# Kernel tuning notes

Measured on AMD Instinct MI355X. Metric: run time of the kernel, lower is better.

## Reference

```python
import jax, jax.numpy as jnp
import numpy as np

EPS = 1e-5

def _conv1x1(x, W, b):
    # x: [B,Ci,H,W], W: [Co,Ci]
    return jnp.einsum('oi,bihw->bohw', W, x) + b[None, :, None, None]

def _bn(x, gamma, beta, mean, var):
    # inference-mode BatchNorm2d
    s = gamma / jnp.sqrt(var + EPS)
    return x * s[None, :, None, None] + (beta - mean * s)[None, :, None, None]

def _conv3x3(x, W, b):
    y = jax.lax.conv_general_dilated(x, W, (1, 1), 'SAME',
                                     dimension_numbers=('NCHW', 'OIHW', 'NCHW'))
    return y + b[None, :, None, None]

def _sparsemax_last(S):
    # sparsemax over the last axis (TrackHSPA: max-subtract, sort, cumsum, threshold)
    S = S - jnp.max(S, axis=-1, keepdims=True)
    srt = -jnp.sort(-S, axis=-1)                 # descending sort
    csum = jnp.cumsum(srt, axis=-1) - 1.0
    N = S.shape[-1]
    ar = jnp.arange(1, N + 1, dtype=S.dtype)
    mask = ar * srt > csum
    k = jnp.sum(mask, axis=-1, keepdims=True)    # support size per row
    tau = jnp.take_along_axis(csum, k - 1, axis=-1) / k.astype(S.dtype)
    return jnp.maximum(S - tau, 0.0)

def _forward(zf, xf, Wq, bq, Ws, bs, Wg, bg, g_gamma, g_beta, g_mean, g_var,
             Wfi, bfi, fi_gamma, fi_beta, fi_mean, fi_var,
             Wm, bm, m_gamma, m_beta, m_mean, m_var, prelu_a):
    B, C, Hx, Wx = xf.shape
    # ---- Graph_Attention_Union (cross-attention) ----
    xf_t = _conv1x1(xf, Wq, bq).reshape(B, C, -1)      # [B,C,Nx]
    zf_t = _conv1x1(zf, Ws, bs).reshape(B, C, -1)      # [B,C,Nz]
    xf_g = jax.nn.relu(_bn(_conv1x1(xf, Wg, bg), g_gamma, g_beta, g_mean, g_var))
    zf_g = jax.nn.relu(_bn(_conv1x1(zf, Wg, bg), g_gamma, g_beta, g_mean, g_var))
    sim = jnp.einsum('bcn,bcm->bnm', xf_t, zf_t)       # [B,Nx,Nz]
    attn = jax.nn.softmax(sim, axis=2)
    emb = jnp.einsum('bcm,bnm->bcn', zf_g.reshape(B, C, -1), attn)
    emb = emb.reshape(B, C, Hx, Wx)
    gat = jax.nn.relu(_bn(_conv1x1(jnp.concatenate([emb, xf_g], axis=1), Wfi, bfi),
                          fi_gamma, fi_beta, fi_mean, fi_var))
    # ---- TrackHSPA (adaptive sparsemax self-attention) ----
    e = _conv3x3(gat, Wm, bm)
    e = _bn(e, m_gamma, m_beta, m_mean, m_var)
    e = jnp.where(e >= 0, e, prelu_a * e)              # PReLU (single param)
    N = Hx * Wx
    ef = e.reshape(B, -1, N)                           # [B,C',N]
    S = jnp.einsum('bdi,bdj->bij', ef, ef)             # [B,N,N]
    P = _sparsemax_last(S)
    out = jnp.einsum('bcn,bnm->bcm', gat.reshape(B, C, N), P)
    return out.reshape(B, C, Hx, Wx) + gat


def setup_inputs():
    key = jax.random.key(0)
    ks = jax.random.split(key, 8)
    B, C, Hz, Wz, Hx, Wx = 32, 256, 7, 7, 31, 31
    Cm = C // 4
    f = lambda k, shape: jax.random.normal(k, shape, jnp.float32) * 0.05
    return {
        'zf': jax.random.normal(ks[0], (B, C, Hz, Wz), jnp.float32),
        'xf': jax.random.normal(ks[1], (B, C, Hx, Wx), jnp.float32),
        'Wq': f(ks[2], (C, C)), 'bq': jnp.zeros((C,), jnp.float32),
        'Ws': f(ks[3], (C, C)), 'bs': jnp.zeros((C,), jnp.float32),
        'Wg': f(ks[4], (C, C)), 'bg': jnp.zeros((C,), jnp.float32),
        'g_gamma': jnp.ones((C,), jnp.float32), 'g_beta': jnp.zeros((C,), jnp.float32),
        'g_mean': jnp.zeros((C,), jnp.float32), 'g_var': jnp.ones((C,), jnp.float32),
        'Wfi': f(ks[5], (C, 2 * C)), 'bfi': jnp.zeros((C,), jnp.float32),
        'fi_gamma': jnp.ones((C,), jnp.float32), 'fi_beta': jnp.zeros((C,), jnp.float32),
        'fi_mean': jnp.zeros((C,), jnp.float32), 'fi_var': jnp.ones((C,), jnp.float32),
        'Wm': f(ks[6], (Cm, C, 3, 3)), 'bm': jnp.zeros((Cm,), jnp.float32),
        'm_gamma': jnp.ones((Cm,), jnp.float32), 'm_beta': jnp.zeros((Cm,), jnp.float32),
        'm_mean': jnp.zeros((Cm,), jnp.float32), 'm_var': jnp.ones((Cm,), jnp.float32),
        'prelu_a': jnp.array(0.25, jnp.float32),
    }


def reference(zf, xf, Wq, bq, Ws, bs, Wg, bg, g_gamma, g_beta, g_mean, g_var,
              Wfi, bfi, fi_gamma, fi_beta, fi_mean, fi_var,
              Wm, bm, m_gamma, m_beta, m_mean, m_var, prelu_a):
    return _forward(zf, xf, Wq, bq, Ws, bs, Wg, bg, g_gamma, g_beta, g_mean, g_var,
                    Wfi, bfi, fi_gamma, fi_beta, fi_mean, fi_var,
                    Wm, bm, m_gamma, m_beta, m_mean, m_var, prelu_a)
```

## Files before the change

### kernel.cpp

```cpp
#include <hip/hip_runtime.h>
#include <cstdint>
#include <cstddef>
#include <math.h>

typedef __attribute__((ext_vector_type(8))) short short8;
typedef __attribute__((ext_vector_type(4))) float floatx4;
typedef unsigned short ushort_t;

__device__ __forceinline__ ushort_t f2bf(float x) {
    union { float f; unsigned u; } v; v.f = x;
    unsigned r = v.u + 0x7FFF + ((v.u >> 16) & 1);
    return (ushort_t)(r >> 16);
}
__device__ __forceinline__ float bf2f(ushort_t h) {
    union { unsigned u; float f; } v; v.u = ((unsigned)h) << 16; return v.f;
}
__device__ __forceinline__ void split2(float v, ushort_t& h, ushort_t& l) {
    h = f2bf(v);
    l = f2bf(v - bf2f(h));
}

#define MFMA(a, b, c) __builtin_amdgcn_mfma_f32_16x16x32_bf16((a), (b), (c), 0, 0, 0)

__device__ __forceinline__ void gload_lds16(const void* g, void* l) {
    __builtin_amdgcn_global_load_lds(
        (const __attribute__((address_space(1))) unsigned*)g,
        (__attribute__((address_space(3))) unsigned*)l, 16, 0, 0);
}

__global__ void prep_all_kernel(
    const float* __restrict__ Wq, const float* __restrict__ Ws,
    const float* __restrict__ Wg, const float* __restrict__ Wfi,
    const float* __restrict__ Wm,
    const float* bq, const float* bs,
    const float* bg, const float* gg, const float* gb, const float* gm, const float* gv,
    const float* bfi, const float* fg, const float* fb, const float* fm, const float* fv,
    const float* bm, const float* mg, const float* mb, const float* mm, const float* mv,
    ushort_t* Wq_h, ushort_t* Wq_l, ushort_t* Ws_h, ushort_t* Ws_l,
    ushort_t* Wg_h, ushort_t* Wg_l, ushort_t* Wfi_h, ushort_t* Wfi_l,
    ushort_t* wm_h, ushort_t* wm_l, float* scsh)
{
    int bid = blockIdx.x, t = threadIdx.x;
    if (bid < 256) {
        int i = bid * 256 + t; ushort_t h, l; split2(Wq[i], h, l); Wq_h[i] = h; Wq_l[i] = l;
    } else if (bid < 512) {
        int i = (bid - 256) * 256 + t; ushort_t h, l; split2(Ws[i], h, l); Ws_h[i] = h; Ws_l[i] = l;
    } else if (bid < 768) {
        int i = (bid - 512) * 256 + t; ushort_t h, l; split2(Wg[i], h, l); Wg_h[i] = h; Wg_l[i] = l;
    } else if (bid < 1280) {
        int i = (bid - 768) * 256 + t; ushort_t h, l; split2(Wfi[i], h, l); Wfi_h[i] = h; Wfi_l[i] = l;
    } else if (bid < 1856) {
        int i = (bid - 1280) * 256 + t;
        int c = i & 255, m = (i >> 8) & 63, tap = i >> 14;
        ushort_t h, l; split2(Wm[((size_t)m * 256 + c) * 9 + tap], h, l);
        wm_h[i] = h; wm_l[i] = l;
    } else {
        if (t < 256) {
            scsh[t] = 1.f;        scsh[256 + t] = bq[t];
            scsh[512 + t] = 1.f;  scsh[768 + t] = bs[t];
            float s = gg[t] * rsqrtf(gv[t] + 1e-5f);
            scsh[1024 + t] = s;   scsh[1280 + t] = gb[t] + s * (bg[t] - gm[t]);
            float s2 = fg[t] * rsqrtf(fv[t] + 1e-5f);
            scsh[1536 + t] = s2;  scsh[1792 + t] = fb[t] + s2 * (bfi[t] - fm[t]);
            if (t < 64) {
                float s3 = mg[t] * rsqrtf(mv[t] + 1e-5f);
                scsh[2048 + t] = s3; scsh[2112 + t] = mb[t] + s3 * (bm[t] - mm[t]);
            }
        }
    }
}

__global__ void halo_zero_kernel(ushort_t* __restrict__ gxh, ushort_t* __restrict__ gxl) {
    int i = blockIdx.x * 256 + threadIdx.x;
    int b = i >> 7, k = i & 127;
    int r;
    if (k < 33) r = k;
    else if (k < 66) r = 32 * 33 + (k - 33);
    else { int k2 = k - 66; r = ((k2 >> 1) + 1) * 33 + ((k2 & 1) ? 32 : 0); }
    uint4* ph = (uint4*)(gxh + ((size_t)b * 1089 + r) * 256);
    uint4* pl = (uint4*)(gxl + ((size_t)b * 1089 + r) * 256);
    uint4 z = make_uint4(0, 0, 0, 0);
#pragma unroll
    for (int s = 0; s < 32; s++) { ph[s] = z; pl[s] = z; }
}

__global__ __launch_bounds__(256) void transpose_in_kernel(
    const float* __restrict__ in, ushort_t* __restrict__ oh, ushort_t* __restrict__ ol,
    int Nsrc, int Npad)
{
    int b = blockIdx.z;
    const float* ib = in + (size_t)b * 256 * Nsrc;
    ushort_t* obh = oh + (size_t)b * Npad * 256;
    ushort_t* obl = ol + (size_t)b * Npad * 256;
    __shared__ float tile[32][33];
    int n0 = blockIdx.x * 32, c0 = blockIdx.y * 32;
    int tx = threadIdx.x & 31, ty = threadIdx.x >> 5;
#pragma unroll
    for (int r = 0; r < 4; r++) {
        int c = c0 + ty + r * 8, n = n0 + tx;
        tile[ty + r * 8][tx] = (n < Nsrc) ? ib[(size_t)c * Nsrc + n] : 0.f;
    }
    __syncthreads();
#pragma unroll
    for (int r = 0; r < 4; r++) {
        int n = n0 + ty + r * 8, c = c0 + tx;
        if (n < Nsrc) {
            ushort_t h, l; split2(tile[tx][ty + r * 8], h, l);
            obh[(size_t)n * 256 + c] = h;
            obl[(size_t)n * 256 + c] = l;
        }
    }
}

__global__ __launch_bounds__(256, 2) void dualconv_mfma_kernel(
    const ushort_t* __restrict__ Xh, const ushort_t* __restrict__ Xl,
    const ushort_t* __restrict__ W1h, const ushort_t* __restrict__ W1l,
    const ushort_t* __restrict__ W2h, const ushort_t* __restrict__ W2l,
    const float* __restrict__ sc1, const float* __restrict__ sh1,
    const float* __restrict__ sc2, const float* __restrict__ sh2,
    int relu1, int relu2,
    ushort_t* __restrict__ O1h, ushort_t* __restrict__ O1l,
    ushort_t* __restrict__ O2h, ushort_t* __restrict__ O2l,
    ushort_t* __restrict__ O2ch, ushort_t* __restrict__ O2cl, int cpitch,
    int K, int Nvalid, int NpadIn, int NpadOut)
{
    __shared__ ushort_t Bs[16384];
    int b = blockIdx.x;
    int n0 = blockIdx.y * 32;
    const ushort_t* Xbh = Xh + (size_t)b * NpadIn * K;
    const ushort_t* Xbl = Xl + (size_t)b * NpadIn * K;
    int tid = threadIdx.x, w = tid >> 6, l = tid & 63, lc = l & 15, q = l >> 4;
    int m0 = w * 64;

#pragma unroll
    for (int r = 0; r < 8; r++) {
        int d = r * 4096 + w * 1024 + l * 16;
        int seg = d >> 14;
        int dr = d & 16383;
        int row = dr >> 9;
        int inrow = (dr & 511) ^ ((row & 7) << 4);
        int srow = n0 + row; if (srow > NpadIn - 1) srow = NpadIn - 1;
        const ushort_t* src = (seg ? Xbl : Xbh) + (size_t)srow * K + (inrow >> 1);
        char* dst = (char*)Bs + (r * 4096 + w * 1024);
        gload_lds16(src, dst);
    }
    __syncthreads();

#define DC_LOADA(K0, AH, AL) do { \
    _Pragma("unroll") \
    for (int mt_ = 0; mt_ < 4; mt_++) { \
        size_t off_ = (size_t)(m0 + mt_ * 16 + lc) * K + (K0) + q * 8; \
        AH[mt_] = *(const short8*)(Wh + off_); \
        AL[mt_] = *(const short8*)(Wl + off_); \
    } \
} while (0)
#define DC_LDSB(K0, BH, BL) do { \
    _Pragma("unroll") \
    for (int jt_ = 0; jt_ < 2; jt_++) { \
        int row_ = jt_ * 16 + lc; \
        int koff_ = (((K0) + q * 8) * 2) ^ ((row_ & 7) << 4); \
        BH[jt_] = *(const short8*)((const char*)Bs + row_ * 512 + koff_); \
        BL[jt_] = *(const short8*)((const char*)Bs + 16384 + row_ * 512 + koff_); \
    } \
} while (0)
#define DC_MFMA(AH, AL, BH, BL) do { \
    _Pragma("unroll") \
    for (int mt_ = 0; mt_ < 4; mt_++) \
    _Pragma("unroll") \
    for (int jt_ = 0; jt_ < 2; jt_++) { \
        acc[mt_][jt_] = MFMA(AH[mt_], BH[jt_], acc[mt_][jt_]); \
        acc[mt_][jt_] = MFMA(AH[mt_], BL[jt_], acc[mt_][jt_]); \
        acc[mt_][jt_] = MFMA(AL[mt_], BH[jt_], acc[mt_][jt_]); \
    } \
} while (0)

    for (int half = 0; half < 2; half++) {
        const ushort_t* Wh = half ? W2h : W1h;
        const ushort_t* Wl = half ? W2l : W1l;
        const float* sc = half ? sc2 : sc1;
        const float* sh = half ? sh2 : sh1;
        int relu = half ? relu2 : relu1;
        ushort_t* Obh = (half ? O2h : O1h) + (size_t)b * NpadOut * 256;
        ushort_t* Obl = (half ? O2l : O1l) + (size_t)b * NpadOut * 256;

        floatx4 acc[4][2];
#pragma unroll
        for (int i = 0; i < 4; i++)
#pragma unroll
            for (int j = 0; j < 2; j++) acc[i][j] = (floatx4){0.f, 0.f, 0.f, 0.f};

        short8 ah0[4], al0[4], ah1[4], al1[4], bh[2], bl[2];
        DC_LOADA(0, ah0, al0);
        for (int k0 = 0; k0 < K; k0 += 64) {
            DC_LOADA(k0 + 32, ah1, al1);
            DC_LDSB(k0, bh, bl);
            DC_MFMA(ah0, al0, bh, bl);
            if (k0 + 64 < K) DC_LOADA(k0 + 64, ah0, al0);
            DC_LDSB(k0 + 32, bh, bl);
            DC_MFMA(ah1, al1, bh, bl);
        }

#pragma unroll
        for (int mt = 0; mt < 4; mt++) {
            int mb = m0 + mt * 16 + q * 4;
            float s0 = sc[mb], s1 = sc[mb + 1], s2 = sc[mb + 2], s3 = sc[mb + 3];
            float h0 = sh[mb], h1 = sh[mb + 1], h2 = sh[mb + 2], h3 = sh[mb + 3];
#pragma unroll
            for (int jt = 0; jt < 2; jt++) {
                int n = n0 + jt * 16 + lc;
                if (n >= Nvalid) continue;
                float v0 = acc[mt][jt][0] * s0 + h0;
                float v1 = acc[mt][jt][1] * s1 + h1;
                float v2 = acc[mt][jt][2] * s2 + h2;
                float v3 = acc[mt][jt][3] * s3 + h3;
                if (relu) { v0 = fmaxf(v0, 0.f); v1 = fmaxf(v1, 0.f); v2 = fmaxf(v2, 0.f); v3 = fmaxf(v3, 0.f); }
                ushort_t e0, f0, e1, f1, e2, f2, e3, f3;
                split2(v0, e0, f0); split2(v1, e1, f1); split2(v2, e2, f2); split2(v3, e3, f3);
                *(ushort4*)(Obh + (size_t)n * 256 + mb) = make_ushort4(e0, e1, e2, e3);
                *(ushort4*)(Obl + (size_t)n * 256 + mb) = make_ushort4(f0, f1, f2, f3);
                if (half && O2ch) {
                    O2ch[((size_t)b * 256 + mb + 0) * cpitch + n] = e0;
                    O2ch[((size_t)b * 256 + mb + 1) * cpitch + n] = e1;
                    O2ch[((size_t)b * 256 + mb + 2) * cpitch + n] = e2;
                    O2ch[((size_t)b * 256 + mb + 3) * cpitch + n] = e3;
                    O2cl[((size_t)b * 256 + mb + 0) * cpitch + n] = f0;
                    O2cl[((size_t)b * 256 + mb + 1) * cpitch + n] = f1;
                    O2cl[((size_t)b * 256 + mb + 2) * cpitch + n] = f2;
                    O2cl[((size_t)b * 256 + mb + 3) * cpitch + n] = f3;
                }
            }
        }
    }
#undef DC_LOADA
#undef DC_LDSB
#undef DC_MFMA
}

__global__ __launch_bounds__(256) void attn_mfma_kernel(
    const ushort_t* __restrict__ xth, const ushort_t* __restrict__ xtl,
    const ushort_t* __restrict__ zth, const ushort_t* __restrict__ ztl,
    const ushort_t* __restrict__ zgh, const ushort_t* __restrict__ zgl,
    ushort_t* __restrict__ eh, ushort_t* __restrict__ el)
{
    __shared__ float S[64][68];
    __shared__ ushort_t awh[64][72], awl[64][72];
    __shared__ float T[4][16][20];
    int b = blockIdx.x, n0 = blockIdx.y * 64;
    int tid = threadIdx.x, w = tid >> 6, l = tid & 63, lc = l & 15, q = l >> 4;
    const ushort_t* xhb = xth + (size_t)b * 992 * 256;
    const ushort_t* xlb = xtl + (size_t)b * 992 * 256;
    const ushort_t* zhb = zth + (size_t)b * 64 * 256;
    const ushort_t* zlb = ztl + (size_t)b * 64 * 256;
    const ushort_t* ghb = zgh + (size_t)b * 256 * 64;
    const ushort_t* glb = zgl + (size_t)b * 256 * 64;

    int rowg = n0 + w * 16 + lc;
#pragma unroll
    for (int ct = 0; ct < 4; ct++) {
        floatx4 acc = (floatx4){0.f, 0.f, 0.f, 0.f};
        for (int k0 = 0; k0 < 256; k0 += 32) {
            short8 ah = *(const short8*)(xhb + (size_t)rowg * 256 + k0 + q * 8);
            short8 al = *(const short8*)(xlb + (size_t)rowg * 256 + k0 + q * 8);
            short8 bh = *(const short8*)(zhb + (size_t)(ct * 16 + lc) * 256 + k0 + q * 8);
            short8 bl = *(const short8*)(zlb + (size_t)(ct * 16 + lc) * 256 + k0 + q * 8);
            acc = MFMA(ah, bh, acc);
            acc = MFMA(ah, bl, acc);
            acc = MFMA(al, bh, acc);
        }
#pragma unroll
        for (int r = 0; r < 4; r++) S[w * 16 + q * 4 + r][ct * 16 + lc] = acc[r];
    }
    __syncthreads();
    if (tid < 64) {
        float mx = -INFINITY;
        for (int m = 0; m < 49; m++) mx = fmaxf(mx, S[tid][m]);
        float sum = 0.f;
        for (int m = 0; m < 49; m++) { float e = __expf(S[tid][m] - mx); S[tid][m] = e; sum += e; }
        float inv = 1.f / sum;
        for (int m = 0; m < 64; m++) {
            float vv = (m < 49) ? S[tid][m] * inv : 0.f;
            ushort_t hh, ll; split2(vv, hh, ll);
            awh[tid][m] = hh; awl[tid][m] = ll;
        }
    }
    __syncthreads();
    int nw = l >> 2, cg = l & 3;
#pragma unroll
    for (int ct = 0; ct < 16; ct++) {
        floatx4 acc = (floatx4){0.f, 0.f, 0.f, 0.f};
#pragma unroll
        for (int k0 = 0; k0 < 64; k0 += 32) {
            short8 ah = *(const short8*)(&awh[w * 16 + lc][k0 + q * 8]);
            short8 al = *(const short8*)(&awl[w * 16 + lc][k0 + q * 8]);
            short8 bh = *(const short8*)(ghb + (size_t)(ct * 16 + lc) * 64 + k0 + q * 8);
            short8 bl = *(const short8*)(glb + (size_t)(ct * 16 + lc) * 64 + k0 + q * 8);
            acc = MFMA(ah, bh, acc);
            acc = MFMA(ah, bl, acc);
            acc = MFMA(al, bh, acc);
        }
#pragma unroll
        for (int r = 0; r < 4; r++) T[w][q * 4 + r][lc] = acc[r];
        float4 vv = *(const float4*)&T[w][nw][cg * 4];
        int n = n0 + w * 16 + nw;
        if (n < 961) {
            ushort_t h0, l0, h1, l1, h2, l2_, h3, l3;
            split2(vv.x, h0, l0); split2(vv.y, h1, l1);
            split2(vv.z, h2, l2_); split2(vv.w, h3, l3);
            size_t off = ((size_t)b * 992 + n) * 256 + ct * 16 + cg * 4;
            *(ushort4*)(eh + off) = make_ushort4(h0, h1, h2, h3);
            *(ushort4*)(el + off) = make_ushort4(l0, l1, l2_, l3);
        }
    }
}

__global__ __launch_bounds__(256, 2) void fi_mfma_kernel(
    const ushort_t* __restrict__ Eh, const ushort_t* __restrict__ El,
    const ushort_t* __restrict__ Gh, const ushort_t* __restrict__ Gl,
    const ushort_t* __restrict__ Wh, const ushort_t* __restrict__ Wl,
    const float* __restrict__ sc, const float* __restrict__ sh,
    ushort_t* __restrict__ gxh, ushort_t* __restrict__ gxl,
    ushort_t* __restrict__ gat_nf)
{
    __shared__ ushort_t Bs[16384];
    int b = blockIdx.x;
    const ushort_t* Ebh = Eh + (size_t)b * 992 * 256;
    const ushort_t* Ebl = El + (size_t)b * 992 * 256;
    const ushort_t* Gbh = Gh + (size_t)b * 992 * 256;
    const ushort_t* Gbl = Gl + (size_t)b * 992 * 256;
    ushort_t* gxhb = gxh + (size_t)b * 1089 * 256;
    ushort_t* gxlb = gxl + (size_t)b * 1089 * 256;
    ushort_t* gn = gat_nf + (size_t)b * 256 * 992;
    int tid = threadIdx.x, w = tid >> 6, l = tid & 63, lc = l & 15, q = l >> 4;
    int m0 = w * 64, nb0 = blockIdx.y * 32;

    floatx4 acc[4][2];
#pragma unroll
    for (int i = 0; i < 4; i++)
#pragma unroll
        for (int j = 0; j < 2; j++) acc[i][j] = (floatx4){0.f, 0.f, 0.f, 0.f};

#define FI_LOADA(K0, AH, AL) do { \
    _Pragma("unroll") \
    for (int mt_ = 0; mt_ < 4; mt_++) { \
        size_t off_ = (size_t)(m0 + mt_ * 16 + lc) * 512 + (K0) + q * 8; \
        AH[mt_] = *(const short8*)(Wh + off_); \
        AL[mt_] = *(const short8*)(Wl + off_); \
    } \
} while (0)
#define FI_LDSB(K0, BH, BL) do { \
    _Pragma("unroll") \
    for (int jt_ = 0; jt_ < 2; jt_++) { \
        int row_ = jt_ * 16 + lc; \
        int koff_ = (((K0) + q * 8) * 2) ^ ((row_ & 7) << 4); \
        BH[jt_] = *(const short8*)((const char*)Bs + row_ * 512 + koff_); \
        BL[jt_] = *(const short8*)((const char*)Bs + 16384 + row_ * 512 + koff_); \
    } \
} while (0)
#define FI_MFMA(AH, AL, BH, BL) do { \
    _Pragma("unroll") \
    for (int mt_ = 0; mt_ < 4; mt_++) \
    _Pragma("unroll") \
    for (int jt_ = 0; jt_ < 2; jt_++) { \
        acc[mt_][jt_] = MFMA(AH[mt_], BH[jt_], acc[mt_][jt_]); \
        acc[mt_][jt_] = MFMA(AH[mt_], BL[jt_], acc[mt_][jt_]); \
        acc[mt_][jt_] = MFMA(AL[mt_], BH[jt_], acc[mt_][jt_]); \
    } \
} while (0)

    for (int p = 0; p < 2; p++) {
        const ushort_t* srcH = p ? Gbh : Ebh;
        const ushort_t* srcL = p ? Gbl : Ebl;
        if (p) __syncthreads();
#pragma unroll
        for (int r = 0; r < 8; r++) {
            int d = r * 4096 + w * 1024 + l * 16;
            int seg = d >> 14;
            int dr = d & 16383;
            int row = dr >> 9;
            int inrow = (dr & 511) ^ ((row & 7) << 4);
            int srow = nb0 + row; if (srow > 991) srow = 991;
            const ushort_t* src = (seg ? srcL : srcH) + (size_t)srow * 256 + (inrow >> 1);
            char* dst = (char*)Bs + (r * 4096 + w * 1024);
            gload_lds16(src, dst);
        }
        __syncthreads();

        int pb = p * 256;
        short8 ah0[4], al0[4], ah1[4], al1[4], bh[2], bl[2];
        FI_LOADA(pb, ah0, al0);
        for (int kk = 0; kk < 256; kk += 64) {
            FI_LOADA(pb + kk + 32, ah1, al1);
            FI_LDSB(kk, bh, bl);
            FI_MFMA(ah0, al0, bh, bl);
            if (kk + 64 < 256) FI_LOADA(pb + kk + 64, ah0, al0);
            FI_LDSB(kk + 32, bh, bl);
            FI_MFMA(ah1, al1, bh, bl);
        }
    }
#undef FI_LOADA
#undef FI_LDSB
#undef FI_MFMA

#pragma unroll
    for (int mt = 0; mt < 4; mt++) {
        int mb = m0 + mt * 16 + q * 4;
        float s0 = sc[mb], s1 = sc[mb + 1], s2 = sc[mb + 2], s3 = sc[mb + 3];
        float h0 = sh[mb], h1 = sh[mb + 1], h2 = sh[mb + 2], h3 = sh[mb + 3];
#pragma unroll
        for (int jt = 0; jt < 2; jt++) {
            int n = nb0 + jt * 16 + lc;
            if (n >= 961) continue;
            float v0 = fmaxf(acc[mt][jt][0] * s0 + h0, 0.f);
            float v1 = fmaxf(acc[mt][jt][1] * s1 + h1, 0.f);
            float v2 = fmaxf(acc[mt][jt][2] * s2 + h2, 0.f);
            float v3 = fmaxf(acc[mt][jt][3] * s3 + h3, 0.f);
            ushort_t a0, b0, a1, b1, a2, b2, a3, b3;
            split2(v0, a0, b0); split2(v1, a1, b1); split2(v2, a2, b2); split2(v3, a3, b3);
            int hh = n / 31, ww2 = n - hh * 31;
            int row = (hh + 1) * 33 + (ww2 + 1);
            *(ushort4*)(gxhb + (size_t)row * 256 + mb) = make_ushort4(a0, a1, a2, a3);
            *(ushort4*)(gxlb + (size_t)row * 256 + mb) = make_ushort4(b0, b1, b2, b3);
            gn[(size_t)(mb + 0) * 992 + n] = a0;
            gn[(size_t)(mb + 1) * 992 + n] = a1;
            gn[(size_t)(mb + 2) * 992 + n] = a2;
            gn[(size_t)(mb + 3) * 992 + n] = a3;
        }
    }
}

__global__ __launch_bounds__(256, 2) void conv3x3_mfma_kernel(
    const ushort_t* __restrict__ gxh, const ushort_t* __restrict__ gxl,
    const ushort_t* __restrict__ wmh, const ushort_t* __restrict__ wml,
    const float* __restrict__ sc, const float* __restrict__ sh,
    const float* __restrict__ prelu_a,
    ushort_t* __restrict__ eh, ushort_t* __restrict__ el)
{
    __shared__ float Sp[4][2048];
    int b = blockIdx.x;
    const ushort_t* gxhb = gxh + (size_t)b * 1089 * 256;
    const ushort_t* gxlb = gxl + (size_t)b * 1089 * 256;
    ushort_t* ebh = eh + (size_t)b * 1024 * 64;
    ushort_t* ebl = el + (size_t)b * 1024 * 64;
    int tid = threadIdx.x, w = tid >> 6, l = tid & 63, lc = l & 15, q = l >> 4;
    int j0 = blockIdx.y * 64;

    int base[4];
#pragma unroll
    for (int jt = 0; jt < 4; jt++) {
        int j = j0 + jt * 16 + lc; if (j > 960) j = 960;
        int hh = j / 31, ww2 = j - hh * 31;
        base[jt] = (hh + 1) * 33 + (ww2 + 1);
    }

    floatx4 acc[4][4];
#pragma unroll
    for (int i = 0; i < 4; i++)
#pragma unroll
        for (int j = 0; j < 4; j++) acc[i][j] = (floatx4){0.f, 0.f, 0.f, 0.f};

#define C3_LOAD(SL, AH, AL, BH, BL) do { \
    int sl_ = (SL); \
    int tap_ = (sl_ >= 9) ? sl_ - 9 : sl_; \
    int k0_ = (w * 2 + ((sl_ >= 9) ? 1 : 0)) * 32; \
    int doff_ = (tap_ / 3 - 1) * 33 + (tap_ % 3 - 1); \
    const ushort_t* wth_ = wmh + tap_ * 16384; \
    const ushort_t* wtl_ = wml + tap_ * 16384; \
    _Pragma("unroll") \
    for (int mt_ = 0; mt_ < 4; mt_++) { \
        size_t off_ = (size_t)(mt_ * 16 + lc) * 256 + k0_ + q * 8; \
        AH[mt_] = *(const short8*)(wth_ + off_); \
        AL[mt_] = *(const short8*)(wtl_ + off_); \
    } \
    _Pragma("unroll") \
    for (int jt_ = 0; jt_ < 4; jt_++) { \
        size_t off_ = (size_t)(base[jt_] + doff_) * 256 + k0_ + q * 8; \
        BH[jt_] = *(const short8*)(gxhb + off_); \
        BL[jt_] = *(const short8*)(gxlb + off_); \
    } \
} while (0)
#define C3_MFMA(AH, AL, BH, BL) do { \
    _Pragma("unroll") \
    for (int mt_ = 0; mt_ < 4; mt_++) \
    _Pragma("unroll") \
    for (int jt_ = 0; jt_ < 4; jt_++) { \
        acc[mt_][jt_] = MFMA(AH[mt_], BH[jt_], acc[mt_][jt_]); \
        acc[mt_][jt_] = MFMA(AH[mt_], BL[jt_], acc[mt_][jt_]); \
        acc[mt_][jt_] = MFMA(AL[mt_], BH[jt_], acc[mt_][jt_]); \
    } \
} while (0)

    short8 A0h[4], A0l[4], B0h[4], B0l[4];
    short8 A1h[4], A1l[4], B1h[4], B1l[4];
    C3_LOAD(0, A0h, A0l, B0h, B0l);
#pragma unroll
    for (int it = 0; it < 9; it++) {
        C3_LOAD(it * 2 + 1, A1h, A1l, B1h, B1l);
        C3_MFMA(A0h, A0l, B0h, B0l);
        if (it < 8) C3_LOAD(it * 2 + 2, A0h, A0l, B0h, B0l);
        C3_MFMA(A1h, A1l, B1h, B1l);
    }
#undef C3_LOAD
#undef C3_MFMA

    float pa = prelu_a[0];
#pragma unroll
    for (int ph = 0; ph < 2; ph++) {
        __syncthreads();
#pragma unroll
        for (int mt = 0; mt < 4; mt++)
#pragma unroll
            for (int jt = 0; jt < 2; jt++)
#pragma unroll
                for (int r = 0; r < 4; r++)
                    Sp[w][(mt * 16 + q * 4 + r) * 32 + jt * 16 + lc] = acc[mt][ph * 2 + jt][r];
        __syncthreads();
#pragma unroll
        for (int gi = 0; gi < 2; gi++) {
            int g = tid + gi * 256;
            int j = g & 31, mg = g >> 5;
            int m = mg * 4;
            int jj = j0 + ph * 32 + j;
            if (jj >= 961) continue;
            float v[4];
#pragma unroll
            for (int i = 0; i < 4; i++) {
                int idx = (m + i) * 32 + j;
                v[i] = Sp[0][idx] + Sp[1][idx] + Sp[2][idx] + Sp[3][idx];
                v[i] = v[i] * sc[m + i] + sh[m + i];
                v[i] = v[i] >= 0.f ? v[i] : pa * v[i];
            }
            ushort_t a0, b0, a1, b1, a2, b2, a3, b3;
            split2(v[0], a0, b0); split2(v[1], a1, b1);
            split2(v[2], a2, b2); split2(v[3], a3, b3);
            *(ushort4*)(ebh + (size_t)jj * 64 + m) = make_ushort4(a0, a1, a2, a3);
            *(ushort4*)(ebl + (size_t)jj * 64 + m) = make_ushort4(b0, b1, b2, b3);
        }
    }
}

__global__ __launch_bounds__(512) void hspa_mfma_kernel(
    const ushort_t* __restrict__ eh, const ushort_t* __restrict__ el,
    ushort_t* __restrict__ PT)
{
    const int PITCH = 978;
    __shared__ float S[8 * 978];
    int b = blockIdx.x, nb = blockIdx.y;
    const ushort_t* ebh = eh + (size_t)b * 1024 * 64;
    const ushort_t* ebl = el + (size_t)b * 1024 * 64;
    ushort_t* Pb = PT + (size_t)b * 1024 * 992;
    int tid = threadIdx.x, w = tid >> 6, l = tid & 63, lc = l & 15, q = l >> 4;
    int n0 = nb * 8;

    short8 a0h = *(const short8*)(ebh + (size_t)(n0 + lc) * 64 + q * 8);
    short8 a0l = *(const short8*)(ebl + (size_t)(n0 + lc) * 64 + q * 8);
    short8 a1h = *(const short8*)(ebh + (size_t)(n0 + lc) * 64 + 32 + q * 8);
    short8 a1l = *(const short8*)(ebl + (size_t)(n0 + lc) * 64 + 32 + q * 8);

    for (int jt = w; jt < 61; jt += 8) {
        int j = jt * 16 + lc;
        short8 b0h = *(const short8*)(ebh + (size_t)j * 64 + q * 8);
        short8 b0l = *(const short8*)(ebl + (size_t)j * 64 + q * 8);
        short8 b1h = *(const short8*)(ebh + (size_t)j * 64 + 32 + q * 8);
        short8 b1l = *(const short8*)(ebl + (size_t)j * 64 + 32 + q * 8);
        floatx4 acc = (floatx4){0.f, 0.f, 0.f, 0.f};
        acc = MFMA(a0h, b0h, acc);
        acc = MFMA(a0h, b0l, acc);
        acc = MFMA(a0l, b0h, acc);
        acc = MFMA(a1h, b1h, acc);
        acc = MFMA(a1h, b1l, acc);
        acc = MFMA(a1l, b1h, acc);
        if (q < 2) {
#pragma unroll
            for (int r = 0; r < 4; r++) S[(q * 4 + r) * PITCH + j] = acc[r];
        }
    }
    __syncthreads();

    int r0 = w;
    float sv0[16];
    float mx0 = -INFINITY;
#pragma unroll
    for (int t = 0; t < 16; t++) {
        int j = l + t * 64;
        float s0 = (j < 961) ? S[r0 * PITCH + j] : -INFINITY;
        sv0[t] = s0;
        mx0 = fmaxf(mx0, s0);
    }
    for (int off = 32; off; off >>= 1) mx0 = fmaxf(mx0, __shfl_xor(mx0, off));
#pragma unroll
    for (int t = 0; t < 16; t++) sv0[t] -= mx0;

    float tau0 = -1.f;
    for (int it = 0; it < 16; it++) {
        float s0 = 0.f, c0 = 0.f;
#pragma unroll
        for (int t = 0; t < 16; t++) {
            if (sv0[t] > tau0) { s0 += sv0[t]; c0 += 1.f; }
        }
        for (int off = 32; off; off >>= 1) {
            s0 += __shfl_xor(s0, off); c0 += __shfl_xor(c0, off);
        }
        float nt0 = (s0 - 1.f) / c0;
        bool conv = (nt0 == tau0);
        tau0 = nt0;
        if (conv) break;
    }
#pragma unroll
    for (int t = 0; t < 16; t++) {
        int j = l + t * 64;
        if (j < 976)
            S[r0 * PITCH + j] = (j < 961) ? fmaxf(sv0[t] - tau0, 0.f) : 0.f;
    }
    __syncthreads();

    for (int j = tid; j < 976; j += 512) {
        union { ushort_t u[8]; uint4 v; } p0;
#pragma unroll
        for (int r = 0; r < 8; r++)  p0.u[r] = f2bf(S[r * PITCH + j]);
        *(uint4*)(Pb + (size_t)j * 992 + n0) = p0.v;
    }
}

__global__ __launch_bounds__(256, 2) void out_mfma_kernel(
    const ushort_t* __restrict__ gat_nf, const ushort_t* __restrict__ PT,
    float* __restrict__ out)
{
    int b = blockIdx.x, jb = blockIdx.y;
    const ushort_t* gb = gat_nf + (size_t)b * 256 * 992;
    const ushort_t* Pb = PT + (size_t)b * 1024 * 992;
    float* ob = out + (size_t)b * 256 * 961;
    int tid = threadIdx.x, w = tid >> 6, l = tid & 63, lc = l & 15, q = l >> 4;
    int m0 = w * 64, j0 = jb * 64;

    floatx4 acc[4][4];
#pragma unroll
    for (int i = 0; i < 4; i++)
#pragma unroll
        for (int j = 0; j < 4; j++) acc[i][j] = (floatx4){0.f, 0.f, 0.f, 0.f};

#define OUT_LOAD(K0, AA, BB) do { \
    _Pragma("unroll") \
    for (int mt_ = 0; mt_ < 4; mt_++) \
        AA[mt_] = *(const short8*)(gb + (size_t)(m0 + mt_ * 16 + lc) * 992 + (K0) + q * 8); \
    _Pragma("unroll") \
    for (int jt_ = 0; jt_ < 4; jt_++) \
        BB[jt_] = *(const short8*)(Pb + (size_t)(j0 + jt_ * 16 + lc) * 992 + (K0) + q * 8); \
} while (0)
#define OUT_MFMA(AA, BB) do { \
    _Pragma("unroll") \
    for (int mt_ = 0; mt_ < 4; mt_++) \
    _Pragma("unroll") \
    for (int jt_ = 0; jt_ < 4; jt_++) \
        acc[mt_][jt_] = MFMA(AA[mt_], BB[jt_], acc[mt_][jt_]); \
} while (0)

    short8 a0[4], b0[4], a1[4], b1[4];
    OUT_LOAD(0, a0, b0);
    for (int k0 = 0; k0 < 960; k0 += 64) {
        OUT_LOAD(k0 + 32, a1, b1);
        OUT_MFMA(a0, b0);
        OUT_LOAD(k0 + 64, a0, b0);
        OUT_MFMA(a1, b1);
    }
    OUT_MFMA(a0, b0);
#undef OUT_LOAD
#undef OUT_MFMA

#pragma unroll
    for (int mt = 0; mt < 4; mt++) {
        int mb = m0 + mt * 16 + q * 4;
#pragma unroll
        for (int jt = 0; jt < 4; jt++) {
            int j = j0 + jt * 16 + lc;
            if (j >= 961) continue;
#pragma unroll
            for (int r = 0; r < 4; r++) {
                float g = bf2f(gb[(size_t)(mb + r) * 992 + j]);
                ob[(size_t)(mb + r) * 961 + j] = acc[mt][jt][r] + g;
            }
        }
    }
}

extern "C" void kernel_launch(void* const* d_in, const int* in_sizes, int n_in,
                              void* d_out, int out_size, void* d_ws, size_t ws_size,
                              hipStream_t stream)
{
    const float* zf      = (const float*)d_in[0];
    const float* xf      = (const float*)d_in[1];
    const float* Wq      = (const float*)d_in[2];
    const float* bq      = (const float*)d_in[3];
    const float* Ws      = (const float*)d_in[4];
    const float* bs      = (const float*)d_in[5];
    const float* Wg      = (const float*)d_in[6];
    const float* bg      = (const float*)d_in[7];
    const float* g_gamma = (const float*)d_in[8];
    const float* g_beta  = (const float*)d_in[9];
    const float* g_mean  = (const float*)d_in[10];
    const float* g_var   = (const float*)d_in[11];
    const float* Wfi     = (const float*)d_in[12];
    const float* bfi     = (const float*)d_in[13];
    const float* fi_gamma= (const float*)d_in[14];
    const float* fi_beta = (const float*)d_in[15];
    const float* fi_mean = (const float*)d_in[16];
    const float* fi_var  = (const float*)d_in[17];
    const float* Wm      = (const float*)d_in[18];
    const float* bm      = (const float*)d_in[19];
    const float* m_gamma = (const float*)d_in[20];
    const float* m_beta  = (const float*)d_in[21];
    const float* m_mean  = (const float*)d_in[22];
    const float* m_var   = (const float*)d_in[23];
    const float* prelu_a = (const float*)d_in[24];
    float* out = (float*)d_out;

    ushort_t* ws = (ushort_t*)d_ws;
    ushort_t* Wq_h  = ws + 0;         ushort_t* Wq_l  = ws + 65536;
    ushort_t* Ws_h  = ws + 131072;    ushort_t* Ws_l  = ws + 196608;
    ushort_t* Wg_h  = ws + 262144;    ushort_t* Wg_l  = ws + 327680;
    ushort_t* Wfi_h = ws + 393216;    ushort_t* Wfi_l = ws + 524288;
    ushort_t* wm_h  = ws + 655360;    ushort_t* wm_l  = ws + 802816;
    ushort_t* XT_h    = ws + 950272;
    ushort_t* XT_l    = ws + 9076736;
    ushort_t* xf_tT_h = ws + 17203200;
    ushort_t* xf_tT_l = ws + 25329664;
    ushort_t* zf_tT_h = ws + 33456128;
    ushort_t* zf_tT_l = ws + 33980416;
    ushort_t* zf_gT_h = ws + 34504704;
    ushort_t* zf_gT_l = ws + 35028992;
    ushort_t* gxT_h   = ws + 17203200;
    ushort_t* gxT_l   = ws + 26124288;
    ushort_t* xf_gT_h = ws + 35553280;
    ushort_t* xf_gT_l = ws + 43679744;
    ushort_t* gat_nf  = ws + 51806208;
    ushort_t* eT_h    = ws + 59932672;
    ushort_t* eT_l    = ws + 62029824;
    ushort_t* PT      = ws + 64126976;
    ushort_t* zfT_h   = ws + 96632832;
    ushort_t* zfT_l   = ws + 97157120;
    float* scsh       = (float*)(ws + 97681408);
    ushort_t* zgC_h   = ws + 97685760;
    ushort_t* zgC_l   = ws + 98210048;
    ushort_t* embT_h = XT_h;
    ushort_t* embT_l = XT_l;

    const float* sc_q  = scsh + 0,    *sh_q  = scsh + 256;
    const float* sc_s  = scsh + 512,  *sh_s  = scsh + 768;
    const float* sc_g  = scsh + 1024, *sh_g  = scsh + 1280;
    const float* sc_fi = scsh + 1536, *sh_fi = scsh + 1792;
    const float* sc_m  = scsh + 2048, *sh_m  = scsh + 2112;

    prep_all_kernel<<<1857, 256, 0, stream>>>(
        Wq, Ws, Wg, Wfi, Wm,
        bq, bs, bg, g_gamma, g_beta, g_mean, g_var,
        bfi, fi_gamma, fi_beta, fi_mean, fi_var,
        bm, m_gamma, m_beta, m_mean, m_var,
        Wq_h, Wq_l, Ws_h, Ws_l, Wg_h, Wg_l, Wfi_h, Wfi_l, wm_h, wm_l, scsh);

    transpose_in_kernel<<<dim3(31, 8, 32), 256, 0, stream>>>(xf, XT_h, XT_l, 961, 992);
    transpose_in_kernel<<<dim3(2, 8, 32), 256, 0, stream>>>(zf, zfT_h, zfT_l, 49, 64);

    dualconv_mfma_kernel<<<dim3(32, 31), 256, 0, stream>>>(
        XT_h, XT_l, Wq_h, Wq_l, Wg_h, Wg_l,
        sc_q, sh_q, sc_g, sh_g, 0, 1,
        xf_tT_h, xf_tT_l, xf_gT_h, xf_gT_l,
        nullptr, nullptr, 0, 256, 961, 992, 992);
    dualconv_mfma_kernel<<<dim3(32, 2), 256, 0, stream>>>(
        zfT_h, zfT_l, Ws_h, Ws_l, Wg_h, Wg_l,
        sc_s, sh_s, sc_g, sh_g, 0, 1,
        zf_tT_h, zf_tT_l, zf_gT_h, zf_gT_l,
        zgC_h, zgC_l, 64, 256, 49, 64, 64);

    attn_mfma_kernel<<<dim3(32, 16), 256, 0, stream>>>(
        xf_tT_h, xf_tT_l, zf_tT_h, zf_tT_l, zgC_h, zgC_l, embT_h, embT_l);

    halo_zero_kernel<<<16, 256, 0, stream>>>(gxT_h, gxT_l);

    fi_mfma_kernel<<<dim3(32, 31), 256, 0, stream>>>(
        embT_h, embT_l, xf_gT_h, xf_gT_l, Wfi_h, Wfi_l, sc_fi, sh_fi,
        gxT_h, gxT_l, gat_nf);

    conv3x3_mfma_kernel<<<dim3(32, 16), 256, 0, stream>>>(
        gxT_h, gxT_l, wm_h, wm_l, sc_m, sh_m, prelu_a, eT_h, eT_l);

    hspa_mfma_kernel<<<dim3(32, 122), 512, 0, stream>>>(eT_h, eT_l, PT);

    out_mfma_kernel<<<dim3(32, 16), 256, 0, stream>>>(gat_nf, PT, out);
}
```

Measured before the change: 639.4 us.

## Process 32 query rows per HSPA block with register-prefetched key tiles

The sparsemax attention kernel now handles 32 query rows per block instead of 8, so each key tile is loaded once and reused across two 16-row MFMA groups, and the grid shrinks from 122 to 31 row blocks. Key tiles are double-buffered in registers while the MFMAs run. The full score tile is kept in accumulators, and each warp runs sparsemax on two rows at once using a shared-memory buffer twice as large. The intent is to cut redundant global loads of the key matrix and raise MFMA density, at the cost of more registers, more LDS and fewer blocks.

```diff
diff --git a/kernel.cpp b/kernel.cpp
--- a/kernel.cpp
+++ b/kernel.cpp
@@ -543,81 +543,135 @@
     ushort_t* __restrict__ PT)
 {
     const int PITCH = 978;
-    __shared__ float S[8 * 978];
+    __shared__ float S[16 * 978];
     int b = blockIdx.x, nb = blockIdx.y;
     const ushort_t* ebh = eh + (size_t)b * 1024 * 64;
     const ushort_t* ebl = el + (size_t)b * 1024 * 64;
     ushort_t* Pb = PT + (size_t)b * 1024 * 992;
     int tid = threadIdx.x, w = tid >> 6, l = tid & 63, lc = l & 15, q = l >> 4;
-    int n0 = nb * 8;
-
-    short8 a0h = *(const short8*)(ebh + (size_t)(n0 + lc) * 64 + q * 8);
-    short8 a0l = *(const short8*)(ebl + (size_t)(n0 + lc) * 64 + q * 8);
-    short8 a1h = *(const short8*)(ebh + (size_t)(n0 + lc) * 64 + 32 + q * 8);
-    short8 a1l = *(const short8*)(ebl + (size_t)(n0 + lc) * 64 + 32 + q * 8);
-
-    for (int jt = w; jt < 61; jt += 8) {
-        int j = jt * 16 + lc;
-        short8 b0h = *(const short8*)(ebh + (size_t)j * 64 + q * 8);
-        short8 b0l = *(const short8*)(ebl + (size_t)j * 64 + q * 8);
-        short8 b1h = *(const short8*)(ebh + (size_t)j * 64 + 32 + q * 8);
-        short8 b1l = *(const short8*)(ebl + (size_t)j * 64 + 32 + q * 8);
-        floatx4 acc = (floatx4){0.f, 0.f, 0.f, 0.f};
-        acc = MFMA(a0h, b0h, acc);
-        acc = MFMA(a0h, b0l, acc);
-        acc = MFMA(a0l, b0h, acc);
-        acc = MFMA(a1h, b1h, acc);
-        acc = MFMA(a1h, b1l, acc);
-        acc = MFMA(a1l, b1h, acc);
-        if (q < 2) {
-#pragma unroll
-            for (int r = 0; r < 4; r++) S[(q * 4 + r) * PITCH + j] = acc[r];
-        }
-    }
-    __syncthreads();
-
-    int r0 = w;
-    float sv0[16];
-    float mx0 = -INFINITY;
-#pragma unroll
-    for (int t = 0; t < 16; t++) {
-        int j = l + t * 64;
-        float s0 = (j < 961) ? S[r0 * PITCH + j] : -INFINITY;
-        sv0[t] = s0;
-        mx0 = fmaxf(mx0, s0);
-    }
-    for (int off = 32; off; off >>= 1) mx0 = fmaxf(mx0, __shfl_xor(mx0, off));
-#pragma unroll
-    for (int t = 0; t < 16; t++) sv0[t] -= mx0;
-
-    float tau0 = -1.f;
-    for (int it = 0; it < 16; it++) {
-        float s0 = 0.f, c0 = 0.f;
+    int n0 = nb * 32;
+
+    short8 Ah[2][2], Al[2][2];
+#pragma unroll
+    for (int g = 0; g < 2; g++)
+#pragma unroll
+        for (int kh = 0; kh < 2; kh++) {
+            size_t off = (size_t)(n0 + g * 16 + lc) * 64 + kh * 32 + q * 8;
+            Ah[g][kh] = *(const short8*)(ebh + off);
+            Al[g][kh] = *(const short8*)(ebl + off);
+        }
+
+    floatx4 acc[2][8];
+#pragma unroll
+    for (int g = 0; g < 2; g++)
+#pragma unroll
+        for (int s = 0; s < 8; s++) acc[g][s] = (floatx4){0.f, 0.f, 0.f, 0.f};
+
+#define HS_LOADB(SLOT, BH0, BL0, BH1, BL1) do { \
+    int jt_ = w + (SLOT) * 8; if (jt_ > 60) jt_ = 60; \
+    size_t o_ = (size_t)(jt_ * 16 + lc) * 64 + q * 8; \
+    BH0 = *(const short8*)(ebh + o_); \
+    BL0 = *(const short8*)(ebl + o_); \
+    BH1 = *(const short8*)(ebh + o_ + 32); \
+    BL1 = *(const short8*)(ebl + o_ + 32); \
+} while (0)
+
+    {
+        short8 b0h[2], b0l[2], b1h[2], b1l[2];
+        HS_LOADB(0, b0h[0], b0l[0], b1h[0], b1l[0]);
+#pragma unroll
+        for (int s = 0; s < 8; s++) {
+            const int cur = s & 1, nxt = cur ^ 1;
+            if (s < 7) HS_LOADB(s + 1, b0h[nxt], b0l[nxt], b1h[nxt], b1l[nxt]);
+#pragma unroll
+            for (int g = 0; g < 2; g++) {
+                floatx4 a = acc[g][s];
+                a = MFMA(Ah[g][0], b0h[cur], a);
+                a = MFMA(Ah[g][0], b0l[cur], a);
+                a = MFMA(Al[g][0], b0h[cur], a);
+                a = MFMA(Ah[g][1], b1h[cur], a);
+                a = MFMA(Ah[g][1], b1l[cur], a);
+                a = MFMA(Al[g][1], b1h[cur], a);
+                acc[g][s] = a;
+            }
+        }
+    }
+#undef HS_LOADB
+
+#pragma unroll
+    for (int g = 0; g < 2; g++) {
+        if (g) __syncthreads();
+#pragma unroll
+        for (int s = 0; s < 8; s++) {
+            int jt = w + s * 8;
+            if (jt < 61) {
+                int j = jt * 16 + lc;
+#pragma unroll
+                for (int r = 0; r < 4; r++)
+                    S[(q * 4 + r) * PITCH + j] = acc[g][s][r];
+            }
+        }
+        __syncthreads();
+
+        int r0 = w * 2, r1 = w * 2 + 1;
+        float sv0[16], sv1[16];
+        float mx0 = -INFINITY, mx1 = -INFINITY;
 #pragma unroll
         for (int t = 0; t < 16; t++) {
-            if (sv0[t] > tau0) { s0 += sv0[t]; c0 += 1.f; }
+            int j = l + t * 64;
+            float s0 = (j < 961) ? S[r0 * PITCH + j] : -INFINITY;
+            float s1 = (j < 961) ? S[r1 * PITCH + j] : -INFINITY;
+            sv0[t] = s0; sv1[t] = s1;
+            mx0 = fmaxf(mx0, s0); mx1 = fmaxf(mx1, s1);
         }
         for (int off = 32; off; off >>= 1) {
-            s0 += __shfl_xor(s0, off); c0 += __shfl_xor(c0, off);
-        }
-        float nt0 = (s0 - 1.f) / c0;
-        bool conv = (nt0 == tau0);
-        tau0 = nt0;
-        if (conv) break;
-    }
-#pragma unroll
-    for (int t = 0; t < 16; t++) {
-        int j = l + t * 64;
-        if (j < 976)
-            S[r0 * PITCH + j] = (j < 961) ? fmaxf(sv0[t] - tau0, 0.f) : 0.f;
-    }
-    __syncthreads();
-
-    for (int j = tid; j < 976; j += 512) {
-        union { ushort_t u[8]; uint4 v; } p0;
-#pragma unroll
-        for (int r = 0; r < 8; r++)  p0.u[r] = f2bf(S[r * PITCH + j]);
-        *(uint4*)(Pb + (size_t)j * 992 + n0) = p0.v;
+            mx0 = fmaxf(mx0, __shfl_xor(mx0, off));
+            mx1 = fmaxf(mx1, __shfl_xor(mx1, off));
+        }
+#pragma unroll
+        for (int t = 0; t < 16; t++) { sv0[t] -= mx0; sv1[t] -= mx1; }
+
+        float tau0 = -1.f, tau1 = -1.f;
+        for (int it = 0; it < 16; it++) {
+            float s0 = 0.f, c0 = 0.f, s1 = 0.f, c1 = 0.f;
+#pragma unroll
+            for (int t = 0; t < 16; t++) {
+                if (sv0[t] > tau0) { s0 += sv0[t]; c0 += 1.f; }
+                if (sv1[t] > tau1) { s1 += sv1[t]; c1 += 1.f; }
+            }
+            for (int off = 32; off; off >>= 1) {
+                s0 += __shfl_xor(s0, off); c0 += __shfl_xor(c0, off);
+                s1 += __shfl_xor(s1, off); c1 += __shfl_xor(c1, off);
+            }
+            float nt0 = (s0 - 1.f) / c0;
+            float nt1 = (s1 - 1.f) / c1;
+            bool conv = (nt0 == tau0) && (nt1 == tau1);
+            tau0 = nt0; tau1 = nt1;
+            if (conv) break;
+        }
+#pragma unroll
+        for (int t = 0; t < 16; t++) {
+            int j = l + t * 64;
+            if (j < 976) {
+                S[r0 * PITCH + j] = (j < 961) ? fmaxf(sv0[t] - tau0, 0.f) : 0.f;
+                S[r1 * PITCH + j] = (j < 961) ? fmaxf(sv1[t] - tau1, 0.f) : 0.f;
+            }
+        }
+        __syncthreads();
+
+        int nbase = n0 + g * 16;
+        if (nbase < 976) {
+            for (int j = tid; j < 976; j += 512) {
+                union { ushort_t u[8]; uint4 v; } p0, p1;
+#pragma unroll
+                for (int r = 0; r < 8; r++)  p0.u[r] = f2bf(S[r * PITCH + j]);
+#pragma unroll
+                for (int r = 0; r < 8; r++)  p1.u[r] = f2bf(S[(8 + r) * PITCH + j]);
+                ushort_t* dst = Pb + (size_t)j * 992 + nbase;
+                *(uint4*)(dst) = p0.v;
+                *(uint4*)(dst + 8) = p1.v;
+            }
+        }
     }
 }
 
@@ -782,7 +836,7 @@
     conv3x3_mfma_kernel<<<dim3(32, 16), 256, 0, stream>>>(
         gxT_h, gxT_l, wm_h, wm_l, sc_m, sh_m, prelu_a, eT_h, eT_l);
 
-    hspa_mfma_kernel<<<dim3(32, 122), 512, 0, stream>>>(eT_h, eT_l, PT);
+    hspa_mfma_kernel<<<dim3(32, 31), 512, 0, stream>>>(eT_h, eT_l, PT);
 
     out_mfma_kernel<<<dim3(32, 16), 256, 0, stream>>>(gat_nf, PT, out);
 }
```

Result: faster. 567.6 us (-11.2%).
